# Optimization experiments

Hardware: AMD Instinct MI355X
Metric: run time of the kernel (lower is better)

## Reference

```python
import jax, jax.numpy as jnp
import numpy as np

B, S, V = 2048, 200, 50257
E, H, EMB = 60, 30, 20  # encode_size, hidden_size, embed_size


def setup_inputs() -> dict:
    key = jax.random.key(0)
    ks = jax.random.split(key, 24)
    emb = jax.random.normal(ks[7], (V, EMB), jnp.float32) * 0.02
    emb = emb.at[3].set(0.0)  # padding_idx=3
    inp = {
        'coverage': jax.random.uniform(ks[0], (B, S), jnp.float32),
        'enc_out': jax.random.normal(ks[1], (B, S, E), jnp.float32),
        'h0': jax.random.normal(ks[2], (1, B, H), jnp.float32),
        'c0': jax.random.normal(ks[3], (1, B, H), jnp.float32),
        'attn': jax.random.uniform(ks[4], (B, S), jnp.float32),
        'dec_input': jax.random.randint(ks[5], (B, 1), 0, V, jnp.int32),
        'enc_inputs': jax.random.randint(ks[6], (B, S), 0, V, jnp.int32),
        'embedding': emb,
        # LSTM (torch gate order i,f,g,o)
        'w_ih': jax.random.normal(ks[8], (4 * H, EMB + E), jnp.float32) * 0.1,
        'w_hh': jax.random.normal(ks[9], (4 * H, H), jnp.float32) * 0.1,
        'b_ih': jax.random.normal(ks[10], (4 * H,), jnp.float32) * 0.1,
        'b_hh': jax.random.normal(ks[11], (4 * H,), jnp.float32) * 0.1,
        # Attention submodule
        'attn_wh_w': jax.random.normal(ks[12], (H, E), jnp.float32) * 0.1,
        'attn_wh_b': jax.random.normal(ks[13], (H,), jnp.float32) * 0.1,
        'attn_ws_w': jax.random.normal(ks[14], (H, H), jnp.float32) * 0.1,
        'attn_ws_b': jax.random.normal(ks[15], (H,), jnp.float32) * 0.1,
        'attn_wc': jax.random.uniform(ks[16], (H,), jnp.float32),
        'attn_v': jax.random.uniform(ks[17], (H,), jnp.float32),
        # pointer-gen params
        'wh': jax.random.uniform(ks[18], (E,), jnp.float32),
        'ws': jax.random.uniform(ks[19], (H,), jnp.float32),
        'wx': jax.random.uniform(ks[20], (EMB,), jnp.float32),
        'v_w': jax.random.normal(ks[21], (V, H), jnp.float32) * 0.02,
        'v_b': jax.random.normal(ks[22], (V,), jnp.float32) * 0.02,
    }
    return inp


def reference(coverage, enc_out, h0, c0, attn, dec_input, enc_inputs, embedding,
              w_ih, w_hh, b_ih, b_hh, attn_wh_w, attn_wh_b, attn_ws_w, attn_ws_b,
              attn_wc, attn_v, wh, ws, wx, v_w, v_b):
    # context = bmm(attn[B,1,S], enc_out[B,S,E]) -> [B,E]
    context = jnp.einsum('bs,bse->be', attn, enc_out)
    embed = embedding[dec_input[:, 0]]              # [B,EMB]
    x = jnp.concatenate([context, embed], axis=-1)  # [B,E+EMB]
    # single-step LSTM (torch gate order i,f,g,o)
    gates = x @ w_ih.T + b_ih + h0[0] @ w_hh.T + b_hh
    i, f, g, o = jnp.split(gates, 4, axis=-1)
    c = jax.nn.sigmoid(f) * c0[0] + jax.nn.sigmoid(i) * jnp.tanh(g)
    h = jax.nn.sigmoid(o) * jnp.tanh(c)             # rnn_out [B,H]
    p_vocab = jax.nn.softmax(h @ v_w.T + v_b, axis=1)   # [B,V]
    p_gen = jax.nn.sigmoid(context @ wh + h @ ws + embed @ wx)[:, None]  # [B,1]
    # attention
    wh_app = enc_out @ attn_wh_w.T + attn_wh_b      # [B,S,H]
    ws_app = (h @ attn_ws_w.T + attn_ws_b)[:, None, :]  # [B,1,H]
    wc_app = coverage[..., None] * attn_wc          # [B,S,H]
    energy = jnp.tanh(wh_app + ws_app + wc_app) @ attn_v  # [B,S]
    new_attn = jax.nn.softmax(energy, axis=1)
    coverage_loss = jnp.sum(jnp.minimum(new_attn, coverage))
    new_coverage = coverage + new_attn
    # scatter copy-attention into vocab space (duplicate idx: arbitrary winner, as torch scatter_)
    rows = jnp.arange(enc_inputs.shape[0])[:, None]
    attn_scores = jnp.zeros((enc_inputs.shape[0], v_w.shape[0]), p_vocab.dtype).at[rows, enc_inputs].set(new_attn)
    output = p_gen * p_vocab + (1.0 - p_gen) * attn_scores
    return output, new_coverage, (h[None], c[None]), new_attn, coverage_loss
```

## Files before the change

kernel.cpp:

```cpp
#include <hip/hip_runtime.h>

#define BB 2048
#define SS 200
#define VV 50257
#define EE 60
#define HH 30
#define EMBD 20
#define XD 80
#define G4 120
#define NCHUNK 100
#define VPAD 51200
#define SROW 132

#define O_COV ((size_t)BB*VV)
#define O_H   (O_COV + (size_t)BB*SS)
#define O_C   (O_H + (size_t)BB*HH)
#define O_NA  (O_C + (size_t)BB*HH)
#define O_LOSS (O_NA + (size_t)BB*SS)

typedef __attribute__((ext_vector_type(8))) short short8v;
typedef __attribute__((ext_vector_type(4))) float f32x4;

__device__ __forceinline__ float sigf(float x){ return 1.f/(1.f+__expf(-x)); }

__device__ __forceinline__ short f2bf(float f){
  union { __bf16 h; short s; } u; u.h = (__bf16)f; return u.s;
}

__device__ __forceinline__ float bsum(float v, float* red, int tid){
  #pragma unroll
  for (int off=32; off; off>>=1) v += __shfl_xor(v, off);
  __syncthreads();
  if ((tid&63)==0) red[tid>>6]=v;
  __syncthreads();
  return red[0]+red[1]+red[2]+red[3];
}
__device__ __forceinline__ float bmax(float v, float* red, int tid){
  #pragma unroll
  for (int off=32; off; off>>=1) v = fmaxf(v, __shfl_xor(v, off));
  __syncthreads();
  if ((tid&63)==0) red[tid>>6]=v;
  __syncthreads();
  return fmaxf(fmaxf(red[0],red[1]),fmaxf(red[2],red[3]));
}

__global__ __launch_bounds__(256) void k_pack(
  const float* __restrict__ v_w, const float* __restrict__ v_b,
  short* __restrict__ vw_bf, float* __restrict__ vb_pad)
{
  const int idx = blockIdx.x*256 + threadIdx.x;
  const int col = idx>>2, q = idx&3;
  union { short8v v; short s[8]; } u;
  #pragma unroll
  for (int j=0;j<8;j++){
    int k = q*8+j;
    u.s[j] = (col<VV && k<HH) ? f2bf(v_w[(size_t)col*HH+k]) : (short)0;
  }
  ((short8v*)vw_bf)[idx] = u.v;
  if (q==0) vb_pad[col] = (col<VV) ? v_b[col] : -1e30f;
}

__global__ __launch_bounds__(256) void k_row(
  const float* __restrict__ coverage, const float* __restrict__ enc_out,
  const float* __restrict__ h0, const float* __restrict__ c0,
  const float* __restrict__ attn, const int* __restrict__ dec_input,
  const float* __restrict__ embedding,
  const float* __restrict__ w_ih, const float* __restrict__ w_hh,
  const float* __restrict__ b_ih, const float* __restrict__ b_hh,
  const float* __restrict__ attn_wh_w, const float* __restrict__ attn_wh_b,
  const float* __restrict__ attn_ws_w, const float* __restrict__ attn_ws_b,
  const float* __restrict__ attn_wc, const float* __restrict__ attn_v,
  const float* __restrict__ whv, const float* __restrict__ wsv, const float* __restrict__ wxv,
  float* __restrict__ out, float* __restrict__ pgen_ws,
  float* __restrict__ losspart_ws, short* __restrict__ h_bf)
{
  const int b = blockIdx.x, tid = threadIdx.x;
  __shared__ float enc[SS*61];
  __shared__ float wT[EE*32];
  __shared__ float attn_s[SS], cov_s[SS];
  __shared__ float xls[XD], hls[HH], wsapp[HH], wc_s[HH], v_s[HH], gls[G4];
  __shared__ float ctxp[EE*4];
  __shared__ float red[4];

  {
    const float4* ep = (const float4*)(enc_out + (size_t)b*(SS*EE));
    #pragma unroll
    for (int it=0; it<12; ++it){
      int i = tid + it*256;
      if (i < (SS*EE/4)) {
        float4 v = ep[i];
        int s = i/15, e4 = (i - s*15)*4;
        float* d = &enc[s*61+e4];
        d[0]=v.x; d[1]=v.y; d[2]=v.z; d[3]=v.w;
      }
    }
  }
  if (tid < SS) { attn_s[tid]=attn[(size_t)b*SS+tid]; cov_s[tid]=coverage[(size_t)b*SS+tid]; }
  for (int i=tid; i<EE*HH; i+=256){ int h=i/EE, e=i-h*EE; wT[e*32+h]=attn_wh_w[i]; }
  if (tid >= 256-HH) { int h = tid-(256-HH); wc_s[h]=attn_wc[h]; v_s[h]=attn_v[h]; }
  __syncthreads();

  if (tid < 240){
    int g = tid/60, e = tid - g*60;
    float acc=0.f;
    for (int s=g; s<SS; s+=4) acc += attn_s[s]*enc[s*61+e];
    ctxp[e*4+g]=acc;
  }
  __syncthreads();
  if (tid < EE) xls[tid]=ctxp[tid*4]+ctxp[tid*4+1]+ctxp[tid*4+2]+ctxp[tid*4+3];
  else if (tid < EE+EMBD){
    int k = tid-EE;
    int dix = dec_input[b];
    xls[tid] = embedding[(size_t)dix*EMBD+k];
  }
  __syncthreads();

  if (tid < G4){
    float acc = b_ih[tid]+b_hh[tid];
    const float* wi = w_ih + tid*XD;
    #pragma unroll
    for (int k=0;k<XD;k++) acc += xls[k]*wi[k];
    const float* whh = w_hh + tid*HH;
    const float* h0b = h0 + (size_t)b*HH;
    #pragma unroll
    for (int k=0;k<HH;k++) acc += h0b[k]*whh[k];
    gls[tid]=acc;
  }
  __syncthreads();
  if (tid < HH){
    float c = sigf(gls[tid+HH])*c0[(size_t)b*HH+tid] + sigf(gls[tid])*tanhf(gls[tid+2*HH]);
    float h = sigf(gls[tid+3*HH])*tanhf(c);
    out[O_C+(size_t)b*HH+tid]=c;
    out[O_H+(size_t)b*HH+tid]=h;
    hls[tid]=h;
  }
  __syncthreads();
  if (tid < 4){
    union { short8v v; short s[8]; } u;
    #pragma unroll
    for (int j=0;j<8;j++){ int k=tid*8+j; u.s[j] = (k<HH)? f2bf(hls[k]) : (short)0; }
    ((short8v*)(h_bf + (size_t)b*32))[tid] = u.v;
  }
  if (tid < HH){
    float acc = attn_ws_b[tid] + attn_wh_b[tid];
    const float* w = attn_ws_w + tid*HH;
    #pragma unroll
    for (int k=0;k<HH;k++) acc += hls[k]*w[k];
    wsapp[tid]=acc;
  }
  float pv=0.f;
  if (tid<EE) pv = xls[tid]*whv[tid];
  else if (tid<EE+HH) pv = hls[tid-EE]*wsv[tid-EE];
  else if (tid<EE+HH+EMBD) pv = xls[EE+(tid-EE-HH)]*wxv[tid-EE-HH];
  float pg = sigf(bsum(pv,red,tid));
  if (tid==0) pgen_ws[b]=pg;
  __syncthreads();

  float en = -1e30f;
  if (tid < SS){
    float acc[HH];
    float cv = cov_s[tid];
    #pragma unroll
    for (int h=0;h<HH;h++) acc[h] = wsapp[h] + cv*wc_s[h];
    for (int e=0;e<EE;e++){
      float evv = enc[tid*61+e];
      #pragma unroll
      for (int h=0;h<HH;h++) acc[h] += evv*wT[e*32+h];
    }
    float e2=0.f;
    #pragma unroll
    for (int h=0;h<HH;h++) e2 += tanhf(acc[h])*v_s[h];
    en = e2;
  }
  float mx = bmax(en, red, tid);
  float ex = (tid<SS)? __expf(en-mx) : 0.f;
  float sm = bsum(ex, red, tid);
  float inv = 1.f/sm;
  float lossv = 0.f;
  if (tid<SS){
    float na = ex*inv;
    float cv = cov_s[tid];
    out[O_NA+(size_t)b*SS+tid]=na;
    out[O_COV+(size_t)b*SS+tid]=cv+na;
    lossv = fminf(na,cv);
  }
  float ls = bsum(lossv,red,tid);
  if (tid==0) losspart_ws[b]=ls;
}

__global__ __launch_bounds__(256) void k_vsum(
  const short* __restrict__ vw_bf, const float* __restrict__ vb_pad,
  const short* __restrict__ h_bf, float* __restrict__ partial)
{
  __shared__ short h_lds[64*32];
  __shared__ float wred[4][64];
  const int tid = threadIdx.x;
  const int rbase = blockIdx.x*64;
  const int cbase = blockIdx.y*512;
  ((uint4*)h_lds)[tid] = ((const uint4*)(h_bf + (size_t)rbase*32))[tid];
  __syncthreads();

  const int w = tid>>6, l = tid&63;
  const int lc = l&15, lg = l>>4;

  short8v Af[4];
  #pragma unroll
  for (int mt=0;mt<4;mt++)
    Af[mt] = *(const short8v*)&h_lds[(mt*16+lc)*32 + lg*8];

  float psum[4][4];
  #pragma unroll
  for (int mt=0;mt<4;mt++)
    #pragma unroll
    for (int r=0;r<4;r++) psum[mt][r]=0.f;

  const int wc0 = cbase + w*128;
  for (int t=0;t<8;t++){
    const int col = wc0 + t*16 + lc;
    short8v Bf = *(const short8v*)(vw_bf + (size_t)col*32 + lg*8);
    const float vb = vb_pad[col];
    #pragma unroll
    for (int mt=0;mt<4;mt++){
      f32x4 z = {0.f,0.f,0.f,0.f};
      f32x4 d = __builtin_amdgcn_mfma_f32_16x16x32_bf16(Af[mt], Bf, z, 0,0,0);
      #pragma unroll
      for (int r=0;r<4;r++) psum[mt][r] += __expf(d[r]+vb);
    }
  }
  #pragma unroll
  for (int mt=0;mt<4;mt++){
    #pragma unroll
    for (int r=0;r<4;r++){
      float s = psum[mt][r];
      s += __shfl_xor(s,1); s += __shfl_xor(s,2); s += __shfl_xor(s,4); s += __shfl_xor(s,8);
      if (lc==0) wred[w][mt*16+lg*4+r]=s;
    }
  }
  __syncthreads();
  if (tid<64)
    partial[(size_t)blockIdx.y*BB + rbase + tid] =
      wred[0][tid]+wred[1][tid]+wred[2][tid]+wred[3][tid];
}

__global__ __launch_bounds__(256) void k_off(
  const float* __restrict__ partial, const float* __restrict__ pgen,
  float* __restrict__ offs)
{
  const int row = blockIdx.x*256 + threadIdx.x;
  float s=0.f;
  #pragma unroll 4
  for (int c=0;c<NCHUNK;c++) s += partial[(size_t)c*BB + row];
  offs[row] = __logf(pgen[row]) - __logf(s);
}

__global__ __launch_bounds__(256) void k_vwrite(
  const short* __restrict__ vw_bf, const float* __restrict__ vb_pad,
  const short* __restrict__ h_bf, const float* __restrict__ offs,
  float* __restrict__ out)
{
  __shared__ short h_lds[16*32];
  __shared__ float stage[4][16*SROW];
  const int tid = threadIdx.x;
  const int rbase = blockIdx.x*16;
  const int cbase = blockIdx.y*2048;
  if (tid < 64) ((uint4*)h_lds)[tid] = ((const uint4*)(h_bf + (size_t)rbase*32))[tid];
  __syncthreads();

  const int w = tid>>6, l = tid&63;
  const int lc = l&15, lg = l>>4;

  short8v Af = *(const short8v*)&h_lds[lc*32 + lg*8];
  float offv[4];
  #pragma unroll
  for (int r=0;r<4;r++) offv[r] = offs[rbase + lg*4 + r];

  float* sw = stage[w];
  const int wc0 = cbase + w*512;

  for (int c=0;c<4;c++){
    const int c0 = wc0 + c*128;
    #pragma unroll
    for (int t=0;t<8;t++){
      const int col = c0 + t*16 + lc;
      short8v Bf = *(const short8v*)(vw_bf + (size_t)col*32 + lg*8);
      const float vb = vb_pad[col];
      f32x4 z = {0.f,0.f,0.f,0.f};
      f32x4 d = __builtin_amdgcn_mfma_f32_16x16x32_bf16(Af, Bf, z, 0,0,0);
      #pragma unroll
      for (int r=0;r<4;r++)
        sw[(lg*4+r)*SROW + t*16 + lc] = __expf(d[r]+vb+offv[r]);
    }
    #pragma unroll 4
    for (int i=0;i<16;i++){
      float* op = out + (size_t)(rbase+i)*VV + c0;
      const float* sp = &sw[i*SROW];
      #pragma unroll
      for (int j=0;j<2;j++){
        const int ci = j*64 + l;
        if (c0 + ci < VV) __builtin_nontemporal_store(sp[ci], &op[ci]);
      }
    }
  }
}

__global__ __launch_bounds__(256) void k_scatter(
  const int* __restrict__ enc_inputs, const float* __restrict__ pgen,
  const float* __restrict__ na, float* __restrict__ out)
{
  __shared__ int idx_s[SS];
  const int b=blockIdx.x, tid=threadIdx.x;
  if (tid<SS) idx_s[tid]=enc_inputs[(size_t)b*SS+tid];
  __syncthreads();
  if (tid<SS){
    int idx=idx_s[tid];
    bool last=true;
    for (int s2=tid+1;s2<SS;s2++) if (idx_s[s2]==idx){ last=false; break; }
    if (last){
      float add=(1.f-pgen[b])*na[(size_t)b*SS+tid];
      out[(size_t)b*VV+idx]+=add;
    }
  }
}

__global__ __launch_bounds__(256) void k_loss(const float* __restrict__ lp, float* __restrict__ dst){
  __shared__ float red[4];
  int tid=threadIdx.x;
  float s=0.f;
  for (int i=tid;i<BB;i+=256) s+=lp[i];
  #pragma unroll
  for (int off=32; off; off>>=1) s+=__shfl_xor(s,off);
  if ((tid&63)==0) red[tid>>6]=s;
  __syncthreads();
  if (tid==0) dst[0]=red[0]+red[1]+red[2]+red[3];
}

extern "C" void kernel_launch(void* const* d_in, const int* in_sizes, int n_in,
                              void* d_out, int out_size, void* d_ws, size_t ws_size,
                              hipStream_t stream)
{
  const float* coverage =(const float*)d_in[0];
  const float* enc_out  =(const float*)d_in[1];
  const float* h0       =(const float*)d_in[2];
  const float* c0       =(const float*)d_in[3];
  const float* attn     =(const float*)d_in[4];
  const int*   dec_input=(const int*)d_in[5];
  const int*   enc_inputs=(const int*)d_in[6];
  const float* embedding=(const float*)d_in[7];
  const float* w_ih     =(const float*)d_in[8];
  const float* w_hh     =(const float*)d_in[9];
  const float* b_ih     =(const float*)d_in[10];
  const float* b_hh     =(const float*)d_in[11];
  const float* attn_wh_w=(const float*)d_in[12];
  const float* attn_wh_b=(const float*)d_in[13];
  const float* attn_ws_w=(const float*)d_in[14];
  const float* attn_ws_b=(const float*)d_in[15];
  const float* attn_wc  =(const float*)d_in[16];
  const float* attn_v   =(const float*)d_in[17];
  const float* whv      =(const float*)d_in[18];
  const float* wsv      =(const float*)d_in[19];
  const float* wxv      =(const float*)d_in[20];
  const float* v_w      =(const float*)d_in[21];
  const float* v_b      =(const float*)d_in[22];
  float* out=(float*)d_out;
  float* wsf=(float*)d_ws;
  float* pgen    = wsf;
  float* losspart= wsf + 2048;
  float* offs    = wsf + 4096;
  float* partial = wsf + 6144;
  float* vb_pad  = wsf + 6144 + (size_t)NCHUNK*BB;
  short* vw_bf   = (short*)(vb_pad + VPAD);
  short* h_bf    = vw_bf + (size_t)VPAD*32;

  k_pack<<<VPAD*4/256,256,0,stream>>>(v_w,v_b,vw_bf,vb_pad);

  k_row<<<BB,256,0,stream>>>(coverage,enc_out,h0,c0,attn,dec_input,embedding,
    w_ih,w_hh,b_ih,b_hh,attn_wh_w,attn_wh_b,attn_ws_w,attn_ws_b,attn_wc,attn_v,
    whv,wsv,wxv,out,pgen,losspart,h_bf);

  dim3 g2(BB/64, NCHUNK);
  k_vsum  <<<g2,256,0,stream>>>(vw_bf,vb_pad,h_bf,partial);
  k_off   <<<BB/256,256,0,stream>>>(partial,pgen,offs);
  dim3 gw(BB/16, VPAD/2048);
  k_vwrite<<<gw,256,0,stream>>>(vw_bf,vb_pad,h_bf,offs,out);
  k_scatter<<<BB,256,0,stream>>>(enc_inputs,pgen,out+O_NA,out);
  k_loss<<<1,256,0,stream>>>(losspart,out+O_LOSS);
}
```

Before: 360.3 us.

## Restructure vocab-sum to per-wave 16-row tasks and shrink vwrite staging chunks

The softmax-denominator kernel now gives each wave an independent task of 16 rows by 1024 vocab columns. The A fragment is read straight from global memory, with no LDS staging, block syncs or cross-wave reduction, and the partial chunk count is halved. The write kernel stages 64-column chunks instead of 128 and uses plain stores instead of nontemporal stores. This trades the old reuse of B fragments across four M tiles for less synchronisation, and dropping nontemporal stores may affect cache behaviour on the large output write.

After: 332.6 us. 1.08x faster.

```diff
diff --git a/kernel.cpp b/kernel.cpp
--- a/kernel.cpp
+++ b/kernel.cpp
@@ -8,9 +8,9 @@
 #define EMBD 20
 #define XD 80
 #define G4 120
-#define NCHUNK 100
+#define NCHUNK 50
 #define VPAD 51200
-#define SROW 132
+#define SROW 68
 
 #define O_COV ((size_t)BB*VV)
 #define O_H   (O_COV + (size_t)BB*SS)
@@ -192,54 +192,34 @@
   const short* __restrict__ vw_bf, const float* __restrict__ vb_pad,
   const short* __restrict__ h_bf, float* __restrict__ partial)
 {
-  __shared__ short h_lds[64*32];
-  __shared__ float wred[4][64];
   const int tid = threadIdx.x;
-  const int rbase = blockIdx.x*64;
-  const int cbase = blockIdx.y*512;
-  ((uint4*)h_lds)[tid] = ((const uint4*)(h_bf + (size_t)rbase*32))[tid];
-  __syncthreads();
-
   const int w = tid>>6, l = tid&63;
   const int lc = l&15, lg = l>>4;
-
-  short8v Af[4];
-  #pragma unroll
-  for (int mt=0;mt<4;mt++)
-    Af[mt] = *(const short8v*)&h_lds[(mt*16+lc)*32 + lg*8];
-
-  float psum[4][4];
-  #pragma unroll
-  for (int mt=0;mt<4;mt++)
-    #pragma unroll
-    for (int r=0;r<4;r++) psum[mt][r]=0.f;
-
-  const int wc0 = cbase + w*128;
-  for (int t=0;t<8;t++){
-    const int col = wc0 + t*16 + lc;
+  const int task = blockIdx.x*4 + w;
+  const int rg = task & 127, cg = task >> 7;
+  const int rbase = rg*16, cbase = cg*1024;
+
+  short8v Af = *(const short8v*)(h_bf + (size_t)(rbase+lc)*32 + lg*8);
+
+  float psum[4] = {0.f,0.f,0.f,0.f};
+  #pragma unroll 4
+  for (int t=0;t<64;t++){
+    const int col = cbase + t*16 + lc;
     short8v Bf = *(const short8v*)(vw_bf + (size_t)col*32 + lg*8);
     const float vb = vb_pad[col];
-    #pragma unroll
-    for (int mt=0;mt<4;mt++){
-      f32x4 z = {0.f,0.f,0.f,0.f};
-      f32x4 d = __builtin_amdgcn_mfma_f32_16x16x32_bf16(Af[mt], Bf, z, 0,0,0);
-      #pragma unroll
-      for (int r=0;r<4;r++) psum[mt][r] += __expf(d[r]+vb);
-    }
-  }
-  #pragma unroll
-  for (int mt=0;mt<4;mt++){
-    #pragma unroll
-    for (int r=0;r<4;r++){
-      float s = psum[mt][r];
-      s += __shfl_xor(s,1); s += __shfl_xor(s,2); s += __shfl_xor(s,4); s += __shfl_xor(s,8);
-      if (lc==0) wred[w][mt*16+lg*4+r]=s;
-    }
-  }
-  __syncthreads();
-  if (tid<64)
-    partial[(size_t)blockIdx.y*BB + rbase + tid] =
-      wred[0][tid]+wred[1][tid]+wred[2][tid]+wred[3][tid];
+    f32x4 z = {0.f,0.f,0.f,0.f};
+    f32x4 d = __builtin_amdgcn_mfma_f32_16x16x32_bf16(Af, Bf, z, 0,0,0);
+    psum[0] += __expf(d[0]+vb);
+    psum[1] += __expf(d[1]+vb);
+    psum[2] += __expf(d[2]+vb);
+    psum[3] += __expf(d[3]+vb);
+  }
+  #pragma unroll
+  for (int r=0;r<4;r++){
+    float s = psum[r];
+    s += __shfl_xor(s,1); s += __shfl_xor(s,2); s += __shfl_xor(s,4); s += __shfl_xor(s,8);
+    if (lc==0) partial[(size_t)cg*BB + rbase + lg*4 + r] = s;
+  }
 }
 
 __global__ __launch_bounds__(256) void k_off(
@@ -248,7 +228,7 @@
 {
   const int row = blockIdx.x*256 + threadIdx.x;
   float s=0.f;
-  #pragma unroll 4
+  #pragma unroll 5
   for (int c=0;c<NCHUNK;c++) s += partial[(size_t)c*BB + row];
   offs[row] = __logf(pgen[row]) - __logf(s);
 }
@@ -277,10 +257,10 @@
   float* sw = stage[w];
   const int wc0 = cbase + w*512;
 
-  for (int c=0;c<4;c++){
-    const int c0 = wc0 + c*128;
-    #pragma unroll
-    for (int t=0;t<8;t++){
+  for (int c=0;c<8;c++){
+    const int c0 = wc0 + c*64;
+    #pragma unroll
+    for (int t=0;t<4;t++){
       const int col = c0 + t*16 + lc;
       short8v Bf = *(const short8v*)(vw_bf + (size_t)col*32 + lg*8);
       const float vb = vb_pad[col];
@@ -292,13 +272,8 @@
     }
     #pragma unroll 4
     for (int i=0;i<16;i++){
-      float* op = out + (size_t)(rbase+i)*VV + c0;
-      const float* sp = &sw[i*SROW];
-      #pragma unroll
-      for (int j=0;j<2;j++){
-        const int ci = j*64 + l;
-        if (c0 + ci < VV) __builtin_nontemporal_store(sp[ci], &op[ci]);
-      }
+      if (c0 + l < VV)
+        out[(size_t)(rbase+i)*VV + c0 + l] = sw[i*SROW + l];
     }
   }
 }
@@ -377,8 +352,7 @@
     w_ih,w_hh,b_ih,b_hh,attn_wh_w,attn_wh_b,attn_ws_w,attn_ws_b,attn_wc,attn_v,
     whv,wsv,wxv,out,pgen,losspart,h_bf);
 
-  dim3 g2(BB/64, NCHUNK);
-  k_vsum  <<<g2,256,0,stream>>>(vw_bf,vb_pad,h_bf,partial);
+  k_vsum  <<<1600,256,0,stream>>>(vw_bf,vb_pad,h_bf,partial);
   k_off   <<<BB/256,256,0,stream>>>(partial,pgen,offs);
   dim3 gw(BB/16, VPAD/2048);
   k_vwrite<<<gw,256,0,stream>>>(vw_bf,vb_pad,h_bf,offs,out);
```
